# Performance work log

Measured on AMD Instinct MI355X. Metric: run time of the kernel, lower is better.

Reference implementation:

```python
import jax, jax.numpy as jnp
import numpy as np

DIM = 768
NUM_HEADS = 12
HEAD_DIM = DIM // NUM_HEADS
SCALE = HEAD_DIM ** -0.5


def setup_inputs() -> dict:
    key = jax.random.key(0)
    k_x, k_qkv, k_pw, k_pb = jax.random.split(key, 4)
    B, N = 8, 1024
    x = jax.random.normal(k_x, (B, N, DIM), dtype=jnp.float32)
    # nn.Linear weights stored [out, in]; qkv_bias=False so no qkv bias
    qkv_w = jax.random.normal(k_qkv, (3 * DIM, DIM), dtype=jnp.float32) * 0.02
    proj_w = jax.random.normal(k_pw, (DIM, DIM), dtype=jnp.float32) * 0.02
    proj_b = jax.random.normal(k_pb, (DIM,), dtype=jnp.float32) * 0.02
    return {"x": x, "qkv_w": qkv_w, "proj_w": proj_w, "proj_b": proj_b}


def reference(x, qkv_w, proj_w, proj_b):
    B, N, C = x.shape
    H, D = NUM_HEADS, HEAD_DIM
    # qkv projection: [B,N,3C] -> [3,B,H,N,D]
    qkv = jnp.einsum('bnc,oc->bno', x, qkv_w)
    qkv = qkv.reshape(B, N, 3, H, D).transpose(2, 0, 3, 1, 4)
    q, k, v = qkv[0], qkv[1], qkv[2]
    # scaled dot-product attention, full materialized scores (as original)
    attn = jnp.einsum('bhnd,bhmd->bhnm', q, k) * SCALE
    attn = jax.nn.softmax(attn, axis=-1)
    out = jnp.einsum('bhnm,bhmd->bhnd', attn, v)  # [B,H,N,D]
    out = out.transpose(0, 2, 1, 3).reshape(B, N, C)
    # output projection
    return jnp.einsum('bnc,oc->bno', out, proj_w) + proj_b
```

## Files before the change

kernel.cpp:

```cpp
#include <hip/hip_runtime.h>
#include <math.h>

constexpr int DIM    = 768;
constexpr int NHEADS = 12;
constexpr int HD     = 64;
constexpr int BATCH  = 8;
constexpr int SEQ    = 1024;
constexpr float SCALE = 0.125f;

typedef __attribute__((ext_vector_type(8))) short short8;
typedef __attribute__((ext_vector_type(4))) float f32x4;

static __device__ __forceinline__ unsigned short f2bf(float f) {
  unsigned int u = __float_as_uint(f);
  return (unsigned short)((u + 0x7fffu + ((u >> 16) & 1u)) >> 16);
}
static __device__ __forceinline__ float bf2f(unsigned short h) {
  return __uint_as_float((unsigned int)h << 16);
}

#define GLLD16(gp, lp) __builtin_amdgcn_global_load_lds(                    \
    (__attribute__((address_space(1))) void*)(gp),                          \
    (__attribute__((address_space(3))) void*)(lp), 16, 0, 0)

__global__ __launch_bounds__(256) void convert_bf(
    const float* __restrict__ src, unsigned short* __restrict__ dst, int n4)
{
  int i = blockIdx.x * 256 + threadIdx.x;
  if (i >= n4) return;
  float4 v = ((const float4*)src)[i];
  ushort4 h;
  h.x = f2bf(v.x); h.y = f2bf(v.y); h.z = f2bf(v.z); h.w = f2bf(v.w);
  ((ushort4*)dst)[i] = h;
}

__global__ __launch_bounds__(256) void decompose_k(
    const float* __restrict__ src, unsigned short* __restrict__ hi,
    unsigned short* __restrict__ lo, int n4)
{
  int i = blockIdx.x * 256 + threadIdx.x;
  if (i >= n4) return;
  float4 v = ((const float4*)src)[i];
  ushort4 h, l;
  h.x = f2bf(v.x); l.x = f2bf(v.x - bf2f(h.x));
  h.y = f2bf(v.y); l.y = f2bf(v.y - bf2f(h.y));
  h.z = f2bf(v.z); l.z = f2bf(v.z - bf2f(h.z));
  h.w = f2bf(v.w); l.w = f2bf(v.w - bf2f(h.w));
  ((ushort4*)hi)[i] = h;
  ((ushort4*)lo)[i] = l;
}

template<int BN, int SEGS, bool QKV_EPI>
__global__ __launch_bounds__(256) void gemm_mfma_glld(
    const unsigned short* __restrict__ A0, const unsigned short* __restrict__ A1,
    const unsigned short* __restrict__ B0, const unsigned short* __restrict__ B1,
    const float* __restrict__ bias,
    unsigned short* __restrict__ q_bf, unsigned short* __restrict__ k_bf,
    unsigned short* __restrict__ v_bf, float* __restrict__ out)
{
  constexpr int K = DIM, BK = 64;
  constexpr int NB = BN / 32;
  __shared__ __align__(16) unsigned short Abuf[128 * BK];
  __shared__ __align__(16) unsigned short Bbuf[BN * BK];

  const int tid  = threadIdx.x;
  const int wave = tid >> 6, lane = tid & 63;
  const int quad = lane >> 4, l16 = lane & 15;
  const int wm = wave >> 1, wn = wave & 1;
  const int m0 = blockIdx.x * 128, n0 = blockIdx.y * BN;

  f32x4 acc[4][NB] = {};

  #pragma unroll 1
  for (int seg = 0; seg < SEGS; ++seg) {
    const unsigned short* Asrc = (seg == 1) ? A1 : A0;
    const unsigned short* Bsrc = (seg == 2) ? B1 : B0;
    const unsigned short* ga = Asrc + (size_t)m0 * K;
    const unsigned short* gb = Bsrc + (size_t)n0 * K;

    #pragma unroll 1
    for (int k0 = 0; k0 < K; k0 += BK) {
      #pragma unroll
      for (int i = 0; i < 4; ++i) {
        int c = i * 256 + tid;
        int row = c >> 3;
        int col = ((c & 7) ^ (row & 7)) * 8;
        GLLD16(ga + (size_t)row * K + k0 + col,
               Abuf + (size_t)(i * 256 + wave * 64) * 8);
      }
      #pragma unroll
      for (int i = 0; i < BN / 32; ++i) {
        int c = i * 256 + tid;
        int row = c >> 3;
        int col = ((c & 7) ^ (row & 7)) * 8;
        GLLD16(gb + (size_t)row * K + k0 + col,
               Bbuf + (size_t)(i * 256 + wave * 64) * 8);
      }
      __syncthreads();

      #pragma unroll
      for (int s = 0; s < 2; ++s) {
        short8 af[4], bfr[NB];
        #pragma unroll
        for (int mb = 0; mb < 4; ++mb) {
          int row = wm * 64 + mb * 16 + l16;
          int cg = (s * 4 + quad) ^ (row & 7);
          af[mb] = *(const short8*)&Abuf[row * BK + cg * 8];
        }
        #pragma unroll
        for (int nb = 0; nb < NB; ++nb) {
          int row = wn * (BN / 2) + nb * 16 + l16;
          int cg = (s * 4 + quad) ^ (row & 7);
          bfr[nb] = *(const short8*)&Bbuf[row * BK + cg * 8];
        }
        #pragma unroll
        for (int mb = 0; mb < 4; ++mb)
          #pragma unroll
          for (int nb = 0; nb < NB; ++nb)
            acc[mb][nb] = __builtin_amdgcn_mfma_f32_16x16x32_bf16(
                af[mb], bfr[nb], acc[mb][nb], 0, 0, 0);
      }
      __syncthreads();
    }
  }

  if (QKV_EPI) {
    #pragma unroll
    for (int nb = 0; nb < NB; ++nb) {
      int n = n0 + wn * (BN / 2) + nb * 16 + l16;
      int t = n / DIM, rem = n % DIM;
      int h = rem >> 6, d = rem & 63;
      unsigned short* dst = (t == 0) ? q_bf : (t == 1) ? k_bf : v_bf;
      #pragma unroll
      for (int mb = 0; mb < 4; ++mb) {
        #pragma unroll
        for (int r = 0; r < 4; ++r) {
          int m = m0 + wm * 64 + mb * 16 + quad * 4 + r;
          int bb = m >> 10, nn = m & 1023;
          dst[(((size_t)(bb * NHEADS + h) << 10) + nn) * HD + d] = f2bf(acc[mb][nb][r]);
        }
      }
    }
  } else {
    #pragma unroll
    for (int nb = 0; nb < NB; ++nb) {
      int n = n0 + wn * (BN / 2) + nb * 16 + l16;
      float bv = bias[n];
      #pragma unroll
      for (int mb = 0; mb < 4; ++mb) {
        #pragma unroll
        for (int r = 0; r < 4; ++r) {
          int m = m0 + wm * 64 + mb * 16 + quad * 4 + r;
          out[(size_t)m * DIM + n] = acc[mb][nb][r] + bv;
        }
      }
    }
  }
}

__global__ __launch_bounds__(256) void flash_attn_mfma(
    const unsigned short* __restrict__ q_bf,
    const unsigned short* __restrict__ k_bf,
    const unsigned short* __restrict__ v_bf,
    unsigned short* __restrict__ attn_hi,
    unsigned short* __restrict__ attn_lo)
{
  constexpr int KT = 64;
  constexpr int LD = HD + 8;
  __shared__ __align__(16) unsigned short Ks[KT][LD];
  __shared__ __align__(16) unsigned short Vt[HD][KT + 8];
  __shared__ __align__(16) unsigned short Ps[4][16][KT + 8];

  const int tid  = threadIdx.x;
  const int wave = tid >> 6;
  const int lane = tid & 63;
  const int quad = lane >> 4;
  const int l16  = lane & 15;
  const int bh   = blockIdx.x;
  const int b    = bh / NHEADS, h = bh % NHEADS;
  const int q0   = blockIdx.y * 64;

  const size_t head_base = (size_t)bh << 16;

  short8 aq[2];
  {
    const unsigned short* qs = q_bf + head_base + (size_t)(q0 + wave * 16 + l16) * HD;
    aq[0] = *(const short8*)&qs[0 * 32 + quad * 8];
    aq[1] = *(const short8*)&qs[1 * 32 + quad * 8];
  }

  short8 bv1;
  {
    short one = (l16 == 0) ? (short)0x3f80 : (short)0;
    #pragma unroll
    for (int j = 0; j < 8; ++j) bv1[j] = one;
  }

  f32x4 Oacc[4] = {};
  f32x4 Lacc = {};

  for (int kt = 0; kt < SEQ / KT; ++kt) {
    {
      const unsigned short* ks = k_bf + head_base + (size_t)kt * KT * HD;
      #pragma unroll
      for (int r = 0; r < 2; ++r) {
        int idx = r * 256 + tid;
        int row = idx >> 3, c8 = (idx & 7) * 8;
        *(uint4*)&Ks[row][c8] = *(const uint4*)&ks[row * HD + c8];
      }
    }
    {
      const unsigned short* vs = v_bf + head_base + (size_t)kt * KT * HD;
      int kp = tid & 31, dg = tid >> 5;
      uint4 lo = *(const uint4*)&vs[(2 * kp) * HD + dg * 8];
      uint4 hi = *(const uint4*)&vs[(2 * kp + 1) * HD + dg * 8];
      const unsigned int* lw = (const unsigned int*)&lo;
      const unsigned int* hw = (const unsigned int*)&hi;
      #pragma unroll
      for (int w = 0; w < 4; ++w) {
        unsigned int e = __builtin_amdgcn_perm(hw[w], lw[w], 0x05040100u);
        unsigned int o = __builtin_amdgcn_perm(hw[w], lw[w], 0x07060302u);
        *(unsigned int*)&Vt[dg * 8 + 2 * w + 0][2 * kp] = e;
        *(unsigned int*)&Vt[dg * 8 + 2 * w + 1][2 * kp] = o;
      }
    }
    __syncthreads();

    f32x4 Sacc[4] = {};
    #pragma unroll
    for (int kb = 0; kb < 4; ++kb) {
      #pragma unroll
      for (int s = 0; s < 2; ++s) {
        short8 bk = *(const short8*)&Ks[kb * 16 + l16][s * 32 + quad * 8];
        Sacc[kb] = __builtin_amdgcn_mfma_f32_16x16x32_bf16(aq[s], bk, Sacc[kb], 0, 0, 0);
      }
    }

    #pragma unroll
    for (int kb = 0; kb < 4; ++kb) {
      #pragma unroll
      for (int i = 0; i < 4; ++i) {
        float p = __expf(Sacc[kb][i] * SCALE);
        Ps[wave][quad * 4 + i][kb * 16 + l16] =
            (unsigned short)(__float_as_uint(p) >> 16);
      }
    }

    short8 pa[2];
    pa[0] = *(const short8*)&Ps[wave][l16][0 * 32 + quad * 8];
    pa[1] = *(const short8*)&Ps[wave][l16][1 * 32 + quad * 8];
    #pragma unroll
    for (int db = 0; db < 4; ++db) {
      #pragma unroll
      for (int s = 0; s < 2; ++s) {
        short8 bv = *(const short8*)&Vt[db * 16 + l16][s * 32 + quad * 8];
        Oacc[db] = __builtin_amdgcn_mfma_f32_16x16x32_bf16(pa[s], bv, Oacc[db], 0, 0, 0);
      }
    }
    #pragma unroll
    for (int s = 0; s < 2; ++s)
      Lacc = __builtin_amdgcn_mfma_f32_16x16x32_bf16(pa[s], bv1, Lacc, 0, 0, 0);

    __syncthreads();
  }

  float linv[4];
  #pragma unroll
  for (int i = 0; i < 4; ++i) {
    float lv = __shfl(Lacc[i], quad << 4, 64);
    linv[i] = 1.f / lv;
  }
  #pragma unroll
  for (int i = 0; i < 4; ++i) {
    int n = q0 + wave * 16 + quad * 4 + i;
    size_t row = ((size_t)(b << 10) + n) * DIM + h * HD;
    #pragma unroll
    for (int db = 0; db < 4; ++db) {
      float val = Oacc[db][i] * linv[i];
      unsigned short hv = f2bf(val);
      attn_hi[row + db * 16 + l16] = hv;
      attn_lo[row + db * 16 + l16] = f2bf(val - bf2f(hv));
    }
  }
}

extern "C" void kernel_launch(void* const* d_in, const int* in_sizes, int n_in,
                              void* d_out, int out_size, void* d_ws, size_t ws_size,
                              hipStream_t stream)
{
  const float* x      = (const float*)d_in[0];
  const float* qkv_w  = (const float*)d_in[1];
  const float* proj_w = (const float*)d_in[2];
  const float* proj_b = (const float*)d_in[3];
  float* out = (float*)d_out;

  const int M = BATCH * SEQ;
  const size_t he = (size_t)BATCH * NHEADS * SEQ * HD;

  unsigned short* q_bf  = (unsigned short*)d_ws;
  unsigned short* k_bf  = q_bf + he;
  unsigned short* v_bf  = k_bf + he;
  unsigned short* x_bf  = v_bf + he;
  unsigned short* qw_bf = x_bf + he;
  unsigned short* pw_hi = qw_bf + (size_t)3 * DIM * DIM;
  unsigned short* pw_lo = pw_hi + (size_t)DIM * DIM;
  unsigned short* a_hi  = pw_lo + (size_t)DIM * DIM;
  unsigned short* a_lo  = a_hi + he;

  int nx4 = M * DIM / 4;
  int nq4 = 3 * DIM * DIM / 4;
  int np4 = DIM * DIM / 4;
  convert_bf<<<(nx4 + 255) / 256, 256, 0, stream>>>(x, x_bf, nx4);
  convert_bf<<<(nq4 + 255) / 256, 256, 0, stream>>>(qkv_w, qw_bf, nq4);
  decompose_k<<<(np4 + 255) / 256, 256, 0, stream>>>(proj_w, pw_hi, pw_lo, np4);

  gemm_mfma_glld<128, 1, true><<<dim3(M / 128, 3 * DIM / 128), 256, 0, stream>>>(
      x_bf, nullptr, qw_bf, nullptr, nullptr, q_bf, k_bf, v_bf, nullptr);

  flash_attn_mfma<<<dim3(BATCH * NHEADS, SEQ / 64), 256, 0, stream>>>(
      q_bf, k_bf, v_bf, a_hi, a_lo);

  gemm_mfma_glld<64, 3, false><<<dim3(M / 128, DIM / 64), 256, 0, stream>>>(
      a_hi, a_lo, pw_hi, pw_lo, proj_b, nullptr, nullptr, nullptr, out);
}
```

Baseline: 217.9 us.

## Store V transposed, use swizzled async LDS loads, fold scale into Q

The QKV GEMM epilogue now writes V in transposed [bh][d][n] layout with vector stores and pre-scales Q by scale*log2(e). That lets attention use exp2 and load K and V tiles straight into LDS with global_load_lds and an XOR swizzle, replacing the register-staged loads and in-kernel V transpose. The three prep kernels are merged into one launch, and the attention grid is reordered so query blocks of the same head are adjacent. The aim is to cut LDS staging work, bank conflicts and launch overhead, at the cost of a strided transposed V store in the GEMM epilogue.

```diff
diff --git a/kernel.cpp b/kernel.cpp
--- a/kernel.cpp
+++ b/kernel.cpp
@@ -7,6 +7,7 @@
 constexpr int BATCH  = 8;
 constexpr int SEQ    = 1024;
 constexpr float SCALE = 0.125f;
+constexpr float QSCALE = 0.18033688011112042f;
 
 typedef __attribute__((ext_vector_type(8))) short short8;
 typedef __attribute__((ext_vector_type(4))) float f32x4;
@@ -23,31 +24,39 @@
     (__attribute__((address_space(1))) void*)(gp),                          \
     (__attribute__((address_space(3))) void*)(lp), 16, 0, 0)
 
-__global__ __launch_bounds__(256) void convert_bf(
-    const float* __restrict__ src, unsigned short* __restrict__ dst, int n4)
+constexpr int NX4 = BATCH * SEQ * DIM / 4;
+constexpr int NQ4 = 3 * DIM * DIM / 4;
+constexpr int NP4 = DIM * DIM / 4;
+
+__global__ __launch_bounds__(256) void prep_all(
+    const float* __restrict__ x, const float* __restrict__ qkv_w,
+    const float* __restrict__ proj_w,
+    unsigned short* __restrict__ x_bf, unsigned short* __restrict__ qw_bf,
+    unsigned short* __restrict__ pw_hi, unsigned short* __restrict__ pw_lo)
 {
-  int i = blockIdx.x * 256 + threadIdx.x;
-  if (i >= n4) return;
-  float4 v = ((const float4*)src)[i];
-  ushort4 h;
-  h.x = f2bf(v.x); h.y = f2bf(v.y); h.z = f2bf(v.z); h.w = f2bf(v.w);
-  ((ushort4*)dst)[i] = h;
-}
-
-__global__ __launch_bounds__(256) void decompose_k(
-    const float* __restrict__ src, unsigned short* __restrict__ hi,
-    unsigned short* __restrict__ lo, int n4)
-{
-  int i = blockIdx.x * 256 + threadIdx.x;
-  if (i >= n4) return;
-  float4 v = ((const float4*)src)[i];
-  ushort4 h, l;
-  h.x = f2bf(v.x); l.x = f2bf(v.x - bf2f(h.x));
-  h.y = f2bf(v.y); l.y = f2bf(v.y - bf2f(h.y));
-  h.z = f2bf(v.z); l.z = f2bf(v.z - bf2f(h.z));
-  h.w = f2bf(v.w); l.w = f2bf(v.w - bf2f(h.w));
-  ((ushort4*)hi)[i] = h;
-  ((ushort4*)lo)[i] = l;
+  int gid = blockIdx.x * 256 + threadIdx.x;
+  if (gid < NX4) {
+    float4 v = ((const float4*)x)[gid];
+    ushort4 h;
+    h.x = f2bf(v.x); h.y = f2bf(v.y); h.z = f2bf(v.z); h.w = f2bf(v.w);
+    ((ushort4*)x_bf)[gid] = h;
+  } else if (gid < NX4 + NQ4) {
+    int i = gid - NX4;
+    float4 v = ((const float4*)qkv_w)[i];
+    ushort4 h;
+    h.x = f2bf(v.x); h.y = f2bf(v.y); h.z = f2bf(v.z); h.w = f2bf(v.w);
+    ((ushort4*)qw_bf)[i] = h;
+  } else if (gid < NX4 + NQ4 + NP4) {
+    int i = gid - NX4 - NQ4;
+    float4 v = ((const float4*)proj_w)[i];
+    ushort4 h, l;
+    h.x = f2bf(v.x); l.x = f2bf(v.x - bf2f(h.x));
+    h.y = f2bf(v.y); l.y = f2bf(v.y - bf2f(h.y));
+    h.z = f2bf(v.z); l.z = f2bf(v.z - bf2f(h.z));
+    h.w = f2bf(v.w); l.w = f2bf(v.w - bf2f(h.w));
+    ((ushort4*)pw_hi)[i] = h;
+    ((ushort4*)pw_lo)[i] = l;
+  }
 }
 
 template<int BN, int SEGS, bool QKV_EPI>
@@ -56,7 +65,7 @@
     const unsigned short* __restrict__ B0, const unsigned short* __restrict__ B1,
     const float* __restrict__ bias,
     unsigned short* __restrict__ q_bf, unsigned short* __restrict__ k_bf,
-    unsigned short* __restrict__ v_bf, float* __restrict__ out)
+    unsigned short* __restrict__ v_t, float* __restrict__ out)
 {
   constexpr int K = DIM, BK = 64;
   constexpr int NB = BN / 32;
@@ -130,14 +139,28 @@
       int n = n0 + wn * (BN / 2) + nb * 16 + l16;
       int t = n / DIM, rem = n % DIM;
       int h = rem >> 6, d = rem & 63;
-      unsigned short* dst = (t == 0) ? q_bf : (t == 1) ? k_bf : v_bf;
-      #pragma unroll
-      for (int mb = 0; mb < 4; ++mb) {
-        #pragma unroll
-        for (int r = 0; r < 4; ++r) {
-          int m = m0 + wm * 64 + mb * 16 + quad * 4 + r;
-          int bb = m >> 10, nn = m & 1023;
-          dst[(((size_t)(bb * NHEADS + h) << 10) + nn) * HD + d] = f2bf(acc[mb][nb][r]);
+      if (t == 2) {
+        #pragma unroll
+        for (int mb = 0; mb < 4; ++mb) {
+          int mb_base = m0 + wm * 64 + mb * 16 + quad * 4;
+          int bb = mb_base >> 10, nn = mb_base & 1023;
+          ushort4 s4;
+          s4.x = f2bf(acc[mb][nb][0]); s4.y = f2bf(acc[mb][nb][1]);
+          s4.z = f2bf(acc[mb][nb][2]); s4.w = f2bf(acc[mb][nb][3]);
+          *(ushort4*)&v_t[(((size_t)(bb * NHEADS + h) * HD + d) << 10) + nn] = s4;
+        }
+      } else {
+        unsigned short* dst = (t == 0) ? q_bf : k_bf;
+        float sc = (t == 0) ? QSCALE : 1.f;
+        #pragma unroll
+        for (int mb = 0; mb < 4; ++mb) {
+          #pragma unroll
+          for (int r = 0; r < 4; ++r) {
+            int m = m0 + wm * 64 + mb * 16 + quad * 4 + r;
+            int bb = m >> 10, nn = m & 1023;
+            dst[(((size_t)(bb * NHEADS + h) << 10) + nn) * HD + d] =
+                f2bf(acc[mb][nb][r] * sc);
+          }
         }
       }
     }
@@ -161,34 +184,29 @@
 __global__ __launch_bounds__(256) void flash_attn_mfma(
     const unsigned short* __restrict__ q_bf,
     const unsigned short* __restrict__ k_bf,
-    const unsigned short* __restrict__ v_bf,
+    const unsigned short* __restrict__ v_t,
     unsigned short* __restrict__ attn_hi,
     unsigned short* __restrict__ attn_lo)
 {
   constexpr int KT = 64;
-  constexpr int LD = HD + 8;
-  __shared__ __align__(16) unsigned short Ks[KT][LD];
-  __shared__ __align__(16) unsigned short Vt[HD][KT + 8];
+  __shared__ __align__(16) unsigned short Ks[KT * HD];
+  __shared__ __align__(16) unsigned short Vs[HD * KT];
   __shared__ __align__(16) unsigned short Ps[4][16][KT + 8];
 
   const int tid  = threadIdx.x;
-  const int wave = tid >> 6;
-  const int lane = tid & 63;
-  const int quad = lane >> 4;
-  const int l16  = lane & 15;
-  const int bh   = blockIdx.x;
-  const int b    = bh / NHEADS, h = bh % NHEADS;
-  const int q0   = blockIdx.y * 64;
-
+  const int wave = tid >> 6, lane = tid & 63;
+  const int quad = lane >> 4, l16 = lane & 15;
+  const int bh = blockIdx.y;
+  const int b = bh / NHEADS, h = bh % NHEADS;
+  const int q0 = blockIdx.x * 64;
   const size_t head_base = (size_t)bh << 16;
 
   short8 aq[2];
   {
     const unsigned short* qs = q_bf + head_base + (size_t)(q0 + wave * 16 + l16) * HD;
-    aq[0] = *(const short8*)&qs[0 * 32 + quad * 8];
-    aq[1] = *(const short8*)&qs[1 * 32 + quad * 8];
-  }
-
+    aq[0] = *(const short8*)&qs[quad * 8];
+    aq[1] = *(const short8*)&qs[32 + quad * 8];
+  }
   short8 bv1;
   {
     short one = (l16 == 0) ? (short)0x3f80 : (short)0;
@@ -200,29 +218,21 @@
   f32x4 Lacc = {};
 
   for (int kt = 0; kt < SEQ / KT; ++kt) {
-    {
-      const unsigned short* ks = k_bf + head_base + (size_t)kt * KT * HD;
-      #pragma unroll
-      for (int r = 0; r < 2; ++r) {
-        int idx = r * 256 + tid;
-        int row = idx >> 3, c8 = (idx & 7) * 8;
-        *(uint4*)&Ks[row][c8] = *(const uint4*)&ks[row * HD + c8];
-      }
-    }
-    {
-      const unsigned short* vs = v_bf + head_base + (size_t)kt * KT * HD;
-      int kp = tid & 31, dg = tid >> 5;
-      uint4 lo = *(const uint4*)&vs[(2 * kp) * HD + dg * 8];
-      uint4 hi = *(const uint4*)&vs[(2 * kp + 1) * HD + dg * 8];
-      const unsigned int* lw = (const unsigned int*)&lo;
-      const unsigned int* hw = (const unsigned int*)&hi;
-      #pragma unroll
-      for (int w = 0; w < 4; ++w) {
-        unsigned int e = __builtin_amdgcn_perm(hw[w], lw[w], 0x05040100u);
-        unsigned int o = __builtin_amdgcn_perm(hw[w], lw[w], 0x07060302u);
-        *(unsigned int*)&Vt[dg * 8 + 2 * w + 0][2 * kp] = e;
-        *(unsigned int*)&Vt[dg * 8 + 2 * w + 1][2 * kp] = o;
-      }
+    const unsigned short* ks = k_bf + head_base + (size_t)kt * KT * HD;
+    const unsigned short* vs = v_t + head_base + (size_t)kt * KT;
+    #pragma unroll
+    for (int i = 0; i < 2; ++i) {
+      int c = i * 256 + tid;
+      int row = c >> 3;
+      int col = ((c & 7) ^ (row & 7)) * 8;
+      GLLD16(ks + (size_t)row * HD + col, Ks + (size_t)(i * 256 + wave * 64) * 8);
+    }
+    #pragma unroll
+    for (int i = 0; i < 2; ++i) {
+      int c = i * 256 + tid;
+      int row = c >> 3;
+      int col = ((c & 7) ^ (row & 7)) * 8;
+      GLLD16(vs + (size_t)row * SEQ + col, Vs + (size_t)(i * 256 + wave * 64) * 8);
     }
     __syncthreads();
 
@@ -231,7 +241,9 @@
     for (int kb = 0; kb < 4; ++kb) {
       #pragma unroll
       for (int s = 0; s < 2; ++s) {
-        short8 bk = *(const short8*)&Ks[kb * 16 + l16][s * 32 + quad * 8];
+        int row = kb * 16 + l16;
+        int slot = (s * 4 + quad) ^ (l16 & 7);
+        short8 bk = *(const short8*)&Ks[row * HD + slot * 8];
         Sacc[kb] = __builtin_amdgcn_mfma_f32_16x16x32_bf16(aq[s], bk, Sacc[kb], 0, 0, 0);
       }
     }
@@ -240,20 +252,22 @@
     for (int kb = 0; kb < 4; ++kb) {
       #pragma unroll
       for (int i = 0; i < 4; ++i) {
-        float p = __expf(Sacc[kb][i] * SCALE);
+        float p = exp2f(Sacc[kb][i]);
         Ps[wave][quad * 4 + i][kb * 16 + l16] =
             (unsigned short)(__float_as_uint(p) >> 16);
       }
     }
 
     short8 pa[2];
-    pa[0] = *(const short8*)&Ps[wave][l16][0 * 32 + quad * 8];
-    pa[1] = *(const short8*)&Ps[wave][l16][1 * 32 + quad * 8];
+    pa[0] = *(const short8*)&Ps[wave][l16][quad * 8];
+    pa[1] = *(const short8*)&Ps[wave][l16][32 + quad * 8];
     #pragma unroll
     for (int db = 0; db < 4; ++db) {
       #pragma unroll
       for (int s = 0; s < 2; ++s) {
-        short8 bv = *(const short8*)&Vt[db * 16 + l16][s * 32 + quad * 8];
+        int row = db * 16 + l16;
+        int slot = (s * 4 + quad) ^ (l16 & 7);
+        short8 bv = *(const short8*)&Vs[row * KT + slot * 8];
         Oacc[db] = __builtin_amdgcn_mfma_f32_16x16x32_bf16(pa[s], bv, Oacc[db], 0, 0, 0);
       }
     }
@@ -299,26 +313,22 @@
 
   unsigned short* q_bf  = (unsigned short*)d_ws;
   unsigned short* k_bf  = q_bf + he;
-  unsigned short* v_bf  = k_bf + he;
-  unsigned short* x_bf  = v_bf + he;
+  unsigned short* v_t   = k_bf + he;
+  unsigned short* x_bf  = v_t + he;
   unsigned short* qw_bf = x_bf + he;
   unsigned short* pw_hi = qw_bf + (size_t)3 * DIM * DIM;
   unsigned short* pw_lo = pw_hi + (size_t)DIM * DIM;
   unsigned short* a_hi  = pw_lo + (size_t)DIM * DIM;
   unsigned short* a_lo  = a_hi + he;
 
-  int nx4 = M * DIM / 4;
-  int nq4 = 3 * DIM * DIM / 4;
-  int np4 = DIM * DIM / 4;
-  convert_bf<<<(nx4 + 255) / 256, 256, 0, stream>>>(x, x_bf, nx4);
-  convert_bf<<<(nq4 + 255) / 256, 256, 0, stream>>>(qkv_w, qw_bf, nq4);
-  decompose_k<<<(np4 + 255) / 256, 256, 0, stream>>>(proj_w, pw_hi, pw_lo, np4);
+  prep_all<<<(NX4 + NQ4 + NP4 + 255) / 256, 256, 0, stream>>>(
+      x, qkv_w, proj_w, x_bf, qw_bf, pw_hi, pw_lo);
 
   gemm_mfma_glld<128, 1, true><<<dim3(M / 128, 3 * DIM / 128), 256, 0, stream>>>(
-      x_bf, nullptr, qw_bf, nullptr, nullptr, q_bf, k_bf, v_bf, nullptr);
-
-  flash_attn_mfma<<<dim3(BATCH * NHEADS, SEQ / 64), 256, 0, stream>>>(
-      q_bf, k_bf, v_bf, a_hi, a_lo);
+      x_bf, nullptr, qw_bf, nullptr, nullptr, q_bf, k_bf, v_t, nullptr);
+
+  flash_attn_mfma<<<dim3(SEQ / 64, BATCH * NHEADS), 256, 0, stream>>>(
+      q_bf, k_bf, v_t, a_hi, a_lo);
 
   gemm_mfma_glld<64, 3, false><<<dim3(M / 128, DIM / 64), 256, 0, stream>>>(
       a_hi, a_lo, pw_hi, pw_lo, proj_b, nullptr, nullptr, nullptr, out);
```

Result: slower. 222.8 us (+2.3%).
